# Kernel tuning notes

Hardware: AMD Instinct MI355X
Metric: run time of the kernel (lower is better)

Reference implementation:

```python
import jax, jax.numpy as jnp
import numpy as np

H = 8          # num heads
DK = 64        # d_model // H
D_MODEL = 512
WIN = 256


def setup_inputs() -> dict:
    key = jax.random.key(0)
    ks = jax.random.split(key, 12)
    B, S = 2, 2048
    mk = lambda k, shape, s=1.0: jax.random.normal(k, shape, dtype=jnp.float32) * s
    inp = {
        "query": mk(ks[0], (B, S, D_MODEL)),
        "key_in": mk(ks[1], (B, S, D_MODEL)),
        "value": mk(ks[2], (B, S, D_MODEL)),
        # nn.Linear(d_model, d_model) weights (out,in) and biases, x4
        "Wq": mk(ks[3], (D_MODEL, D_MODEL), 0.02), "bq": jnp.zeros((D_MODEL,), jnp.float32),
        "Wk": mk(ks[4], (D_MODEL, D_MODEL), 0.02), "bk": jnp.zeros((D_MODEL,), jnp.float32),
        "Wv": mk(ks[5], (D_MODEL, D_MODEL), 0.02), "bv": jnp.zeros((D_MODEL,), jnp.float32),
        "Wo": mk(ks[6], (D_MODEL, D_MODEL), 0.02), "bo": jnp.zeros((D_MODEL,), jnp.float32),
    }
    return inp


def reference(query, key_in, value, Wq, bq, Wk, bk, Wv, bv, Wo, bo):
    B, S, D = query.shape
    scale = np.float32(1.0 / np.sqrt(DK))

    def proj(x, W, b):
        # (B,S,D) -> (B,H,S,DK)
        return (x @ W.T + b).reshape(B, S, H, DK).transpose(0, 2, 1, 3)

    q = proj(query, Wq, bq)
    k = proj(key_in, Wk, bk)
    v = proj(value, Wv, bv)

    # Faithful to naive_masked_matmul: full (B,H,S,S) scores, with entries
    # OUTSIDE the sliding window left at exactly 0.0 (NOT -inf) before softmax.
    scores = jnp.einsum('bhid,bhjd->bhij', q, k) * scale
    idx = jnp.arange(S)
    band = jnp.abs(idx[:, None] - idx[None, :]) <= (WIN // 2)  # (S,S) bool
    scores = jnp.where(band, scores, jnp.float32(0.0))

    p_attn = jax.nn.softmax(scores, axis=-1)
    x = jnp.einsum('bhij,bhjd->bhid', p_attn, v)          # (B,H,S,DK)
    x = x.transpose(0, 2, 1, 3).reshape(B, S, D)          # (B,S,D)
    return x @ Wo.T + bo
```

## Files before the change

### kernel.cpp

```cpp
#include <hip/hip_runtime.h>
#include <hip/hip_bf16.h>

#define SS 2048
#define DD 512
#define HWIN 128

typedef __bf16 bf16x8 __attribute__((ext_vector_type(8)));
typedef unsigned short u16x8 __attribute__((ext_vector_type(8)));
typedef float f32x4 __attribute__((ext_vector_type(4)));

__device__ __forceinline__ unsigned short f2bf(float x) {
    unsigned u = __builtin_bit_cast(unsigned, x);
    return (unsigned short)((u + 0x7fffu + ((u >> 16) & 1u)) >> 16);
}
__device__ __forceinline__ float bf2f(unsigned short s) {
    unsigned u = ((unsigned)s) << 16;
    return __builtin_bit_cast(float, u);
}
__device__ __forceinline__ void split_bf(float x, unsigned short& h, unsigned short& l) {
    h = f2bf(x);
    l = f2bf(x - bf2f(h));
}
__device__ __forceinline__ void split8(float4 f0, float4 f1, u16x8& h, u16x8& l) {
    const float vals[8] = {f0.x, f0.y, f0.z, f0.w, f1.x, f1.y, f1.z, f1.w};
    #pragma unroll
    for (int i = 0; i < 8; ++i) {
        unsigned short hh, ll;
        split_bf(vals[i], hh, ll);
        h[i] = hh;
        l[i] = ll;
    }
}
__device__ __forceinline__ f32x4 mfma16(u16x8 a, u16x8 b, f32x4 c) {
    return __builtin_amdgcn_mfma_f32_16x16x32_bf16(
        __builtin_bit_cast(bf16x8, a), __builtin_bit_cast(bf16x8, b), c, 0, 0, 0);
}
__device__ __forceinline__ void gload16(const unsigned short* g, unsigned short* l) {
    __builtin_amdgcn_global_load_lds(
        (const __attribute__((address_space(1))) unsigned int*)g,
        (__attribute__((address_space(3))) unsigned int*)l, 16, 0, 0);
}

__global__ __launch_bounds__(256) void castW(
    const float* __restrict__ wq, const float* __restrict__ wk,
    const float* __restrict__ wv, const float* __restrict__ wo,
    unsigned short* __restrict__ WP, unsigned short* __restrict__ WoP)
{
    const size_t e0 = ((size_t)blockIdx.x * 256 + threadIdx.x) * 8;
    const float* src; size_t off; unsigned short* dst;
    if      (e0 < 262144) { src = wq; off = e0;          dst = WP + 2 * e0; }
    else if (e0 < 524288) { src = wk; off = e0 - 262144; dst = WP + 2 * e0; }
    else if (e0 < 786432) { src = wv; off = e0 - 524288; dst = WP + 2 * e0; }
    else                  { src = wo; off = e0 - 786432; dst = WoP + 2 * (e0 - 786432); }
    u16x8 h, l;
    split8(*(const float4*)(src + off), *(const float4*)(src + off + 4), h, l);
    *(u16x8*)(dst)     = h;
    *(u16x8*)(dst + 8) = l;
}

__global__ __launch_bounds__(256) void proj_gemm(
    const float* __restrict__ q, const float* __restrict__ k, const float* __restrict__ v,
    const unsigned short* __restrict__ WP,
    const float* __restrict__ bq, const float* __restrict__ bk, const float* __restrict__ bv,
    unsigned short* __restrict__ base,
    unsigned short* __restrict__ VTH, unsigned short* __restrict__ VTL)
{
    const int d = blockIdx.x;
    const int hi = d >> 6, low = d & 63;
    const int x = low >> 3, rsw = low & 7;
    const int g = hi * 8 + rsw;
    const int y = g / 3, z = g - y * 3;

    const float* A = (z == 0) ? q : ((z == 1) ? k : v);
    const unsigned short* Wp = WP + (size_t)z * 524288;
    const float* bias = (z == 0) ? bq : ((z == 1) ? bk : bv);
    unsigned short* OH = base + (size_t)z * 4194304;

    const int m0 = y * 128, n0 = x * 64;

    __shared__ unsigned short Ah[8 * 64 * 8], Al[8 * 64 * 8];
    __shared__ unsigned short Bh[4 * 64 * 8], Bl[4 * 64 * 8];

    const int tid = threadIdx.x, wave = tid >> 6, lane = tid & 63;
    const int lm = lane & 15, lq = lane >> 4;
    const int wm = wave >> 1, wn = wave & 1;
    const int kb = lq * 8;

    f32x4 acc[4][2] = {};

    const int ar0 = m0 + (wave * 2 + 0) * 16 + lm;
    const int ar1 = m0 + (wave * 2 + 1) * 16 + lm;
    const int br  = n0 + wave * 16 + lm;

    unsigned short* aD0h = &Ah[((wave * 2 + 0) * 64 + lane) * 8];
    unsigned short* aD1h = &Ah[((wave * 2 + 1) * 64 + lane) * 8];
    unsigned short* aD0l = &Al[((wave * 2 + 0) * 64 + lane) * 8];
    unsigned short* aD1l = &Al[((wave * 2 + 1) * 64 + lane) * 8];
    unsigned short* bDh  = &Bh[(wave * 64 + lane) * 8];
    unsigned short* bDl  = &Bl[(wave * 64 + lane) * 8];

    for (int k0 = 0; k0 < 512; k0 += 32) {
        const float* p0 = A + (size_t)ar0 * 512 + k0 + kb;
        const float4 f00 = *(const float4*)p0, f01 = *(const float4*)(p0 + 4);
        const float* p1 = A + (size_t)ar1 * 512 + k0 + kb;
        const float4 f10 = *(const float4*)p1, f11 = *(const float4*)(p1 + 4);

        __syncthreads();
        u16x8 a0h, a0l, a1h, a1l;
        split8(f00, f01, a0h, a0l);
        split8(f10, f11, a1h, a1l);
        *(u16x8*)aD0h = a0h; *(u16x8*)aD0l = a0l;
        *(u16x8*)aD1h = a1h; *(u16x8*)aD1l = a1l;
        {
            const unsigned short* pw = Wp + 2 * ((size_t)br * 512 + k0 + kb);
            gload16(pw,     bDh);
            gload16(pw + 8, bDl);
        }
        __syncthreads();

        u16x8 afh[4], afl[4], bfh[2], bfl[2];
        #pragma unroll
        for (int i = 0; i < 4; ++i) {
            afh[i] = *(const u16x8*)&Ah[((wm * 4 + i) * 64 + lane) * 8];
            afl[i] = *(const u16x8*)&Al[((wm * 4 + i) * 64 + lane) * 8];
        }
        #pragma unroll
        for (int j = 0; j < 2; ++j) {
            bfh[j] = *(const u16x8*)&Bh[((wn * 2 + j) * 64 + lane) * 8];
            bfl[j] = *(const u16x8*)&Bl[((wn * 2 + j) * 64 + lane) * 8];
        }
        #pragma unroll
        for (int i = 0; i < 4; ++i)
            #pragma unroll
            for (int j = 0; j < 2; ++j) {
                acc[i][j] = mfma16(afh[i], bfh[j], acc[i][j]);
                acc[i][j] = mfma16(afh[i], bfl[j], acc[i][j]);
                acc[i][j] = mfma16(afl[i], bfh[j], acc[i][j]);
            }
    }

    #pragma unroll
    for (int i = 0; i < 4; ++i)
        #pragma unroll
        for (int j = 0; j < 2; ++j) {
            const int col = n0 + (wn * 2 + j) * 16 + lm;
            const float bv_ = bias[col];
            #pragma unroll
            for (int r = 0; r < 4; ++r) {
                const int row = m0 + (wm * 4 + i) * 16 + lq * 4 + r;
                const float vv = acc[i][j][r] + bv_;
                unsigned short hh, ll;
                split_bf(vv, hh, ll);
                if (z == 2) {
                    const size_t vix =
                        (((size_t)(row >> 11) * 8 + (col >> 6)) * 64 + (col & 63)) * 2048
                        + (row & 2047);
                    VTH[vix] = hh;
                    VTL[vix] = ll;
                } else {
                    OH[(size_t)row * 512 + col] = hh;
                }
            }
        }
}

__global__ __launch_bounds__(256) void out_gemm(
    const unsigned short* __restrict__ XHg, const unsigned short* __restrict__ XLg,
    const unsigned short* __restrict__ WoP, const float* __restrict__ bo,
    float* __restrict__ O)
{
    const int gid = blockIdx.x;
    const int rr = gid & 7, hi = gid >> 3;
    const int nblk = hi & 7, mhi = hi >> 3;
    const int mblk = mhi * 8 + rr;
    const int m0 = mblk * 64, n0 = nblk * 64;

    __shared__ unsigned short Ah[8 * 64 * 8], Al[8 * 64 * 8];
    __shared__ unsigned short Bh[8 * 64 * 8], Bl[8 * 64 * 8];

    const int tid = threadIdx.x, wave = tid >> 6, lane = tid & 63;
    const int lm = lane & 15, lq = lane >> 4;
    const int kb = lq * 8;

    f32x4 acc[4] = {};

    const int arow = m0 + wave * 16 + lm;
    const int brow = n0 + wave * 16 + lm;

    for (int k0 = 0; k0 < 512; k0 += 64) {
        __syncthreads();
        #pragma unroll
        for (int s = 0; s < 2; ++s) {
            gload16(XHg + (size_t)arow * 512 + k0 + s * 32 + kb,
                    &Ah[((s * 4 + wave) * 64 + lane) * 8]);
            gload16(XLg + (size_t)arow * 512 + k0 + s * 32 + kb,
                    &Al[((s * 4 + wave) * 64 + lane) * 8]);
            const unsigned short* pw = WoP + 2 * ((size_t)brow * 512 + k0 + s * 32 + kb);
            gload16(pw,     &Bh[((s * 4 + wave) * 64 + lane) * 8]);
            gload16(pw + 8, &Bl[((s * 4 + wave) * 64 + lane) * 8]);
        }
        __syncthreads();

        #pragma unroll
        for (int s = 0; s < 2; ++s) {
            const u16x8 a_h = *(const u16x8*)&Ah[((s * 4 + wave) * 64 + lane) * 8];
            const u16x8 a_l = *(const u16x8*)&Al[((s * 4 + wave) * 64 + lane) * 8];
            #pragma unroll
            for (int j = 0; j < 4; ++j) {
                const u16x8 b_h = *(const u16x8*)&Bh[((s * 4 + j) * 64 + lane) * 8];
                const u16x8 b_l = *(const u16x8*)&Bl[((s * 4 + j) * 64 + lane) * 8];
                acc[j] = mfma16(a_h, b_h, acc[j]);
                acc[j] = mfma16(a_h, b_l, acc[j]);
                acc[j] = mfma16(a_l, b_h, acc[j]);
            }
        }
    }

    #pragma unroll
    for (int j = 0; j < 4; ++j) {
        const int col = n0 + j * 16 + lm;
        const float bv_ = bo[col];
        #pragma unroll
        for (int r = 0; r < 4; ++r) {
            const int row = m0 + wave * 16 + lq * 4 + r;
            O[(size_t)row * 512 + col] = acc[j][r] + bv_;
        }
    }
}

__global__ __launch_bounds__(256) void vsum_stage1(
    const unsigned short* __restrict__ VTH, const unsigned short* __restrict__ VTL,
    float* __restrict__ partial)
{
    const int bh = blockIdx.x, c = blockIdx.y;
    const int t = threadIdx.x, dd = t & 63, g = t >> 6;
    __shared__ float p[4][64];
    const size_t rb = ((size_t)bh * 64 + dd) * 2048 + c * 64 + g * 16;
    const u16x8 h0 = *(const u16x8*)(VTH + rb), h1 = *(const u16x8*)(VTH + rb + 8);
    const u16x8 l0 = *(const u16x8*)(VTL + rb), l1 = *(const u16x8*)(VTL + rb + 8);
    float acc = 0.f;
    #pragma unroll
    for (int i = 0; i < 8; ++i) acc += bf2f(h0[i]) + bf2f(l0[i]);
    #pragma unroll
    for (int i = 0; i < 8; ++i) acc += bf2f(h1[i]) + bf2f(l1[i]);
    p[g][dd] = acc;
    __syncthreads();
    if (t < 64)
        partial[((size_t)bh * 32 + c) * 64 + t] =
            p[0][t] + p[1][t] + p[2][t] + p[3][t];
}

__global__ __launch_bounds__(64) void vsum_stage2(
    const float* __restrict__ partial, float* __restrict__ VS)
{
    const int bh = blockIdx.x, dd = threadIdx.x;
    float acc = 0.f;
    #pragma unroll 8
    for (int c = 0; c < 32; ++c)
        acc += partial[((size_t)bh * 32 + c) * 64 + dd];
    VS[bh * 64 + dd] = acc;
}

__global__ __launch_bounds__(256) void attn_mfma(
    const unsigned short* __restrict__ QH, const unsigned short* __restrict__ KH,
    const unsigned short* __restrict__ VTH, const float* __restrict__ VS,
    unsigned short* __restrict__ XH, unsigned short* __restrict__ XL)
{
    const int dblk = blockIdx.x;
    const int bhi = dblk >> 8, blow = dblk & 255;
    const int xblk = blow >> 3, rrs = blow & 7;
    const int bh = bhi * 8 + rrs;
    const int h = bh & 7, b = bh >> 3;
    const int i0 = xblk * 64;
    const int tid = threadIdx.x, wave = tid >> 6, lane = tid & 63;
    const int lm = lane & 15, lq = lane >> 4;
    const int kb = lq * 8;

    __shared__ unsigned short KfH[8 * 64 * 8];
    __shared__ unsigned short VfH[8 * 64 * 8];
    __shared__ unsigned short Swh[64][72];

    const size_t qoff = ((size_t)(b * SS + i0 + wave * 16 + lm)) * DD + h * 64 + kb;
    const u16x8 aQ0h = *(const u16x8*)(QH + qoff);
    const u16x8 aQ1h = *(const u16x8*)(QH + qoff + 32);

    f32x4 oacc[4] = {};
    float dacc[4] = {0.f, 0.f, 0.f, 0.f};

    unsigned short* kDh0 = &KfH[((wave * 2 + 0) * 64 + lane) * 8];
    unsigned short* kDh1 = &KfH[((wave * 2 + 1) * 64 + lane) * 8];
    unsigned short* vDh0 = &VfH[((wave * 2 + 0) * 64 + lane) * 8];
    unsigned short* vDh1 = &VfH[((wave * 2 + 1) * 64 + lane) * 8];
    const size_t vrow = ((size_t)bh * 64 + wave * 16 + lm) * 2048;

    for (int jt = 0; jt < 5; ++jt) {
        const int jt0 = i0 - 128 + jt * 64;
        {
            const int jrow = jt0 + wave * 16 + lm;
            const int jrc = min(max(jrow, 0), SS - 1);
            const size_t kgb = ((size_t)(b * SS + jrc)) * DD + h * 64 + kb;
            gload16(KH + kgb,      kDh0);
            gload16(KH + kgb + 32, kDh1);
            const int j0c = min(max(jt0 + kb, 0), SS - 8);
            const int j1c = min(max(jt0 + 32 + kb, 0), SS - 8);
            gload16(VTH + vrow + j0c, vDh0);
            gload16(VTH + vrow + j1c, vDh1);
        }
        __syncthreads();

        #pragma unroll
        for (int js = 0; js < 4; ++js) {
            const int j0 = js * 16;
            const u16x8 bK0h = *(const u16x8*)&KfH[((js * 2 + 0) * 64 + lane) * 8];
            const u16x8 bK1h = *(const u16x8*)&KfH[((js * 2 + 1) * 64 + lane) * 8];
            f32x4 s = {0.f, 0.f, 0.f, 0.f};
            s = mfma16(aQ0h, bK0h, s);
            s = mfma16(aQ1h, bK1h, s);
            const int jg = jt0 + j0 + lm;
            const int iq = i0 + wave * 16 + lq * 4;
            #pragma unroll
            for (int r = 0; r < 4; ++r) {
                const int qi = iq + r;
                const bool in = (jg >= 0) && (jg < SS) &&
                                (jg >= qi - HWIN) && (jg <= qi + HWIN);
                const float w = in ? (__expf(s[r] * 0.125f) - 1.0f) : 0.0f;
                dacc[r] += w;
                Swh[wave * 16 + lq * 4 + r][j0 + lm] = f2bf(w);
            }
        }
        __syncthreads();

        const u16x8 aP0h = *(const u16x8*)&Swh[wave * 16 + lm][kb];
        const u16x8 aP1h = *(const u16x8*)&Swh[wave * 16 + lm][kb + 32];
        #pragma unroll
        for (int s4 = 0; s4 < 4; ++s4) {
            const u16x8 bV0h = *(const u16x8*)&VfH[((s4 * 2 + 0) * 64 + lane) * 8];
            const u16x8 bV1h = *(const u16x8*)&VfH[((s4 * 2 + 1) * 64 + lane) * 8];
            oacc[s4] = mfma16(aP0h, bV0h, oacc[s4]);
            oacc[s4] = mfma16(aP1h, bV1h, oacc[s4]);
        }
        __syncthreads();
    }

    #pragma unroll
    for (int r = 0; r < 4; ++r) {
        float v = dacc[r];
        v += __shfl_xor(v, 1);
        v += __shfl_xor(v, 2);
        v += __shfl_xor(v, 4);
        v += __shfl_xor(v, 8);
        dacc[r] = v + 2048.0f;
    }

    #pragma unroll
    for (int s4 = 0; s4 < 4; ++s4) {
        const float vsv = VS[bh * 64 + s4 * 16 + lm];
        #pragma unroll
        for (int r = 0; r < 4; ++r) {
            const int qrow = i0 + wave * 16 + lq * 4 + r;
            const float x = (oacc[s4][r] + vsv) / dacc[r];
            unsigned short xh, xl;
            split_bf(x, xh, xl);
            const size_t ix = ((size_t)(b * SS + qrow)) * DD + h * 64 + s4 * 16 + lm;
            XH[ix] = xh;
            XL[ix] = xl;
        }
    }
}

extern "C" void kernel_launch(void* const* d_in, const int* in_sizes, int n_in,
                              void* d_out, int out_size, void* d_ws, size_t ws_size,
                              hipStream_t stream)
{
    const float* query  = (const float*)d_in[0];
    const float* key_in = (const float*)d_in[1];
    const float* value  = (const float*)d_in[2];
    const float* Wq = (const float*)d_in[3]; const float* bq = (const float*)d_in[4];
    const float* Wk = (const float*)d_in[5]; const float* bk = (const float*)d_in[6];
    const float* Wv = (const float*)d_in[7]; const float* bv = (const float*)d_in[8];
    const float* Wo = (const float*)d_in[9]; const float* bo = (const float*)d_in[10];

    unsigned short* wsb = (unsigned short*)d_ws;
    unsigned short* QH  = wsb;
    unsigned short* KH  = wsb + 4194304;
    unsigned short* VTH = wsb + 8388608;
    unsigned short* VTL = wsb + 10485760;
    unsigned short* XH  = wsb + 12582912;
    unsigned short* XL  = wsb + 14680064;
    unsigned short* WP  = wsb + 16777216;
    unsigned short* WoP = wsb + 18350080;
    float* part = (float*)((char*)d_ws + 62914560);
    float* VSp  = (float*)((char*)d_ws + 63045632);

    castW<<<512, 256, 0, stream>>>(Wq, Wk, Wv, Wo, WP, WoP);

    proj_gemm<<<768, 256, 0, stream>>>(
        query, key_in, value, WP, bq, bk, bv, QH, VTH, VTL);

    vsum_stage1<<<dim3(16, 32), 256, 0, stream>>>(VTH, VTL, part);
    vsum_stage2<<<16, 64, 0, stream>>>(part, VSp);

    attn_mfma<<<512, 256, 0, stream>>>(QH, KH, VTH, VSp, XH, XL);

    out_gemm<<<512, 256, 0, stream>>>(XH, XL, WoP, bo, (float*)d_out);
}
```

Before: 167.7 us.

## Double-buffer LDS tiles in QKV projection and output GEMMs

```diff
diff --git a/kernel.cpp b/kernel.cpp
--- a/kernel.cpp
+++ b/kernel.cpp
@@ -78,8 +78,8 @@
 
     const int m0 = y * 128, n0 = x * 64;
 
-    __shared__ unsigned short Ah[8 * 64 * 8], Al[8 * 64 * 8];
-    __shared__ unsigned short Bh[4 * 64 * 8], Bl[4 * 64 * 8];
+    __shared__ unsigned short Ah[2 * 4096], Al[2 * 4096];
+    __shared__ unsigned short Bh[2 * 2048], Bl[2 * 2048];
 
     const int tid = threadIdx.x, wave = tid >> 6, lane = tid & 63;
     const int lm = lane & 15, lq = lane >> 4;
@@ -92,42 +92,52 @@
     const int ar1 = m0 + (wave * 2 + 1) * 16 + lm;
     const int br  = n0 + wave * 16 + lm;
 
-    unsigned short* aD0h = &Ah[((wave * 2 + 0) * 64 + lane) * 8];
-    unsigned short* aD1h = &Ah[((wave * 2 + 1) * 64 + lane) * 8];
-    unsigned short* aD0l = &Al[((wave * 2 + 0) * 64 + lane) * 8];
-    unsigned short* aD1l = &Al[((wave * 2 + 1) * 64 + lane) * 8];
-    unsigned short* bDh  = &Bh[(wave * 64 + lane) * 8];
-    unsigned short* bDl  = &Bl[(wave * 64 + lane) * 8];
-
-    for (int k0 = 0; k0 < 512; k0 += 32) {
-        const float* p0 = A + (size_t)ar0 * 512 + k0 + kb;
+    const int aoff0 = ((wave * 2 + 0) * 64 + lane) * 8;
+    const int aoff1 = ((wave * 2 + 1) * 64 + lane) * 8;
+    const int boff  = (wave * 64 + lane) * 8;
+
+    {
+        const float* p0 = A + (size_t)ar0 * 512 + kb;
         const float4 f00 = *(const float4*)p0, f01 = *(const float4*)(p0 + 4);
-        const float* p1 = A + (size_t)ar1 * 512 + k0 + kb;
+        const float* p1 = A + (size_t)ar1 * 512 + kb;
         const float4 f10 = *(const float4*)p1, f11 = *(const float4*)(p1 + 4);
-
-        __syncthreads();
-        u16x8 a0h, a0l, a1h, a1l;
-        split8(f00, f01, a0h, a0l);
-        split8(f10, f11, a1h, a1l);
-        *(u16x8*)aD0h = a0h; *(u16x8*)aD0l = a0l;
-        *(u16x8*)aD1h = a1h; *(u16x8*)aD1l = a1l;
-        {
-            const unsigned short* pw = Wp + 2 * ((size_t)br * 512 + k0 + kb);
-            gload16(pw,     bDh);
-            gload16(pw + 8, bDl);
-        }
-        __syncthreads();
+        const unsigned short* pw = Wp + 2 * ((size_t)br * 512 + kb);
+        gload16(pw,     &Bh[boff]);
+        gload16(pw + 8, &Bl[boff]);
+        u16x8 h0, l0, h1, l1;
+        split8(f00, f01, h0, l0);
+        split8(f10, f11, h1, l1);
+        *(u16x8*)&Ah[aoff0] = h0; *(u16x8*)&Al[aoff0] = l0;
+        *(u16x8*)&Ah[aoff1] = h1; *(u16x8*)&Al[aoff1] = l1;
+    }
+    __syncthreads();
+
+    int cur = 0;
+    for (int t = 0; t < 16; ++t) {
+        const int nxt = cur ^ 1;
+        const bool pf = (t < 15);
+        float4 f00, f01, f10, f11;
+        if (pf) {
+            const int k0n = (t + 1) * 32;
+            const float* p0 = A + (size_t)ar0 * 512 + k0n + kb;
+            f00 = *(const float4*)p0; f01 = *(const float4*)(p0 + 4);
+            const float* p1 = A + (size_t)ar1 * 512 + k0n + kb;
+            f10 = *(const float4*)p1; f11 = *(const float4*)(p1 + 4);
+            const unsigned short* pw = Wp + 2 * ((size_t)br * 512 + k0n + kb);
+            gload16(pw,     &Bh[nxt * 2048 + boff]);
+            gload16(pw + 8, &Bl[nxt * 2048 + boff]);
+        }
 
         u16x8 afh[4], afl[4], bfh[2], bfl[2];
         #pragma unroll
         for (int i = 0; i < 4; ++i) {
-            afh[i] = *(const u16x8*)&Ah[((wm * 4 + i) * 64 + lane) * 8];
-            afl[i] = *(const u16x8*)&Al[((wm * 4 + i) * 64 + lane) * 8];
+            afh[i] = *(const u16x8*)&Ah[cur * 4096 + ((wm * 4 + i) * 64 + lane) * 8];
+            afl[i] = *(const u16x8*)&Al[cur * 4096 + ((wm * 4 + i) * 64 + lane) * 8];
         }
         #pragma unroll
         for (int j = 0; j < 2; ++j) {
-            bfh[j] = *(const u16x8*)&Bh[((wn * 2 + j) * 64 + lane) * 8];
-            bfl[j] = *(const u16x8*)&Bl[((wn * 2 + j) * 64 + lane) * 8];
+            bfh[j] = *(const u16x8*)&Bh[cur * 2048 + ((wn * 2 + j) * 64 + lane) * 8];
+            bfl[j] = *(const u16x8*)&Bl[cur * 2048 + ((wn * 2 + j) * 64 + lane) * 8];
         }
         #pragma unroll
         for (int i = 0; i < 4; ++i)
@@ -137,6 +147,16 @@
                 acc[i][j] = mfma16(afh[i], bfl[j], acc[i][j]);
                 acc[i][j] = mfma16(afl[i], bfh[j], acc[i][j]);
             }
+
+        if (pf) {
+            u16x8 h0, l0, h1, l1;
+            split8(f00, f01, h0, l0);
+            split8(f10, f11, h1, l1);
+            *(u16x8*)&Ah[nxt * 4096 + aoff0] = h0; *(u16x8*)&Al[nxt * 4096 + aoff0] = l0;
+            *(u16x8*)&Ah[nxt * 4096 + aoff1] = h1; *(u16x8*)&Al[nxt * 4096 + aoff1] = l1;
+        }
+        __syncthreads();
+        cur = nxt;
     }
 
     #pragma unroll
@@ -175,8 +195,8 @@
     const int mblk = mhi * 8 + rr;
     const int m0 = mblk * 64, n0 = nblk * 64;
 
-    __shared__ unsigned short Ah[8 * 64 * 8], Al[8 * 64 * 8];
-    __shared__ unsigned short Bh[8 * 64 * 8], Bl[8 * 64 * 8];
+    __shared__ unsigned short Ah[2 * 4096], Al[2 * 4096];
+    __shared__ unsigned short Bh[2 * 4096], Bl[2 * 4096];
 
     const int tid = threadIdx.x, wave = tid >> 6, lane = tid & 63;
     const int lm = lane & 15, lq = lane >> 4;
@@ -187,33 +207,49 @@
     const int arow = m0 + wave * 16 + lm;
     const int brow = n0 + wave * 16 + lm;
 
-    for (int k0 = 0; k0 < 512; k0 += 64) {
-        __syncthreads();
+    #pragma unroll
+    for (int s = 0; s < 2; ++s) {
+        const int o = ((s * 4 + wave) * 64 + lane) * 8;
+        gload16(XHg + (size_t)arow * 512 + s * 32 + kb, &Ah[o]);
+        gload16(XLg + (size_t)arow * 512 + s * 32 + kb, &Al[o]);
+        const unsigned short* pw = WoP + 2 * ((size_t)brow * 512 + s * 32 + kb);
+        gload16(pw,     &Bh[o]);
+        gload16(pw + 8, &Bl[o]);
+    }
+    __syncthreads();
+
+    int cur = 0;
+    for (int t = 0; t < 8; ++t) {
+        const int nxt = cur ^ 1;
+        if (t < 7) {
+            const int k0n = (t + 1) * 64;
+            #pragma unroll
+            for (int s = 0; s < 2; ++s) {
+                const int o = nxt * 4096 + ((s * 4 + wave) * 64 + lane) * 8;
+                gload16(XHg + (size_t)arow * 512 + k0n + s * 32 + kb, &Ah[o]);
+                gload16(XLg + (size_t)arow * 512 + k0n + s * 32 + kb, &Al[o]);
+                const unsigned short* pw =
+                    WoP + 2 * ((size_t)brow * 512 + k0n + s * 32 + kb);
+                gload16(pw,     &Bh[o]);
+                gload16(pw + 8, &Bl[o]);
+            }
+        }
+
         #pragma unroll
         for (int s = 0; s < 2; ++s) {
-            gload16(XHg + (size_t)arow * 512 + k0 + s * 32 + kb,
-                    &Ah[((s * 4 + wave) * 64 + lane) * 8]);
-            gload16(XLg + (size_t)arow * 512 + k0 + s * 32 + kb,
-                    &Al[((s * 4 + wave) * 64 + lane) * 8]);
-            const unsigned short* pw = WoP + 2 * ((size_t)brow * 512 + k0 + s * 32 + kb);
-            gload16(pw,     &Bh[((s * 4 + wave) * 64 + lane) * 8]);
-            gload16(pw + 8, &Bl[((s * 4 + wave) * 64 + lane) * 8]);
-        }
-        __syncthreads();
-
-        #pragma unroll
-        for (int s = 0; s < 2; ++s) {
-            const u16x8 a_h = *(const u16x8*)&Ah[((s * 4 + wave) * 64 + lane) * 8];
-            const u16x8 a_l = *(const u16x8*)&Al[((s * 4 + wave) * 64 + lane) * 8];
+            const u16x8 a_h = *(const u16x8*)&Ah[cur * 4096 + ((s * 4 + wave) * 64 + lane) * 8];
+            const u16x8 a_l = *(const u16x8*)&Al[cur * 4096 + ((s * 4 + wave) * 64 + lane) * 8];
             #pragma unroll
             for (int j = 0; j < 4; ++j) {
-                const u16x8 b_h = *(const u16x8*)&Bh[((s * 4 + j) * 64 + lane) * 8];
-                const u16x8 b_l = *(const u16x8*)&Bl[((s * 4 + j) * 64 + lane) * 8];
+                const u16x8 b_h = *(const u16x8*)&Bh[cur * 4096 + ((s * 4 + j) * 64 + lane) * 8];
+                const u16x8 b_l = *(const u16x8*)&Bl[cur * 4096 + ((s * 4 + j) * 64 + lane) * 8];
                 acc[j] = mfma16(a_h, b_h, acc[j]);
                 acc[j] = mfma16(a_h, b_l, acc[j]);
                 acc[j] = mfma16(a_l, b_h, acc[j]);
             }
         }
+        __syncthreads();
+        cur = nxt;
     }
 
     #pragma unroll
```

Result: slower. 173.9 us (+3.7%).

## Replace LDS staging with direct global-to-register loads and register prefetch

Applied to the files above, without the earlier changes.

```diff
diff --git a/kernel.cpp b/kernel.cpp
--- a/kernel.cpp
+++ b/kernel.cpp
@@ -34,11 +34,6 @@
 __device__ __forceinline__ f32x4 mfma16(u16x8 a, u16x8 b, f32x4 c) {
     return __builtin_amdgcn_mfma_f32_16x16x32_bf16(
         __builtin_bit_cast(bf16x8, a), __builtin_bit_cast(bf16x8, b), c, 0, 0, 0);
-}
-__device__ __forceinline__ void gload16(const unsigned short* g, unsigned short* l) {
-    __builtin_amdgcn_global_load_lds(
-        (const __attribute__((address_space(1))) unsigned int*)g,
-        (__attribute__((address_space(3))) unsigned int*)l, 16, 0, 0);
 }
 
 __global__ __launch_bounds__(256) void castW(
@@ -78,9 +73,6 @@
 
     const int m0 = y * 128, n0 = x * 64;
 
-    __shared__ unsigned short Ah[8 * 64 * 8], Al[8 * 64 * 8];
-    __shared__ unsigned short Bh[4 * 64 * 8], Bl[4 * 64 * 8];
-
     const int tid = threadIdx.x, wave = tid >> 6, lane = tid & 63;
     const int lm = lane & 15, lq = lane >> 4;
     const int wm = wave >> 1, wn = wave & 1;
@@ -88,55 +80,61 @@
 
     f32x4 acc[4][2] = {};
 
-    const int ar0 = m0 + (wave * 2 + 0) * 16 + lm;
-    const int ar1 = m0 + (wave * 2 + 1) * 16 + lm;
-    const int br  = n0 + wave * 16 + lm;
-
-    unsigned short* aD0h = &Ah[((wave * 2 + 0) * 64 + lane) * 8];
-    unsigned short* aD1h = &Ah[((wave * 2 + 1) * 64 + lane) * 8];
-    unsigned short* aD0l = &Al[((wave * 2 + 0) * 64 + lane) * 8];
-    unsigned short* aD1l = &Al[((wave * 2 + 1) * 64 + lane) * 8];
-    unsigned short* bDh  = &Bh[(wave * 64 + lane) * 8];
-    unsigned short* bDl  = &Bl[(wave * 64 + lane) * 8];
-
-    for (int k0 = 0; k0 < 512; k0 += 32) {
-        const float* p0 = A + (size_t)ar0 * 512 + k0 + kb;
-        const float4 f00 = *(const float4*)p0, f01 = *(const float4*)(p0 + 4);
-        const float* p1 = A + (size_t)ar1 * 512 + k0 + kb;
-        const float4 f10 = *(const float4*)p1, f11 = *(const float4*)(p1 + 4);
-
-        __syncthreads();
-        u16x8 a0h, a0l, a1h, a1l;
-        split8(f00, f01, a0h, a0l);
-        split8(f10, f11, a1h, a1l);
-        *(u16x8*)aD0h = a0h; *(u16x8*)aD0l = a0l;
-        *(u16x8*)aD1h = a1h; *(u16x8*)aD1l = a1l;
-        {
-            const unsigned short* pw = Wp + 2 * ((size_t)br * 512 + k0 + kb);
-            gload16(pw,     bDh);
-            gload16(pw + 8, bDl);
-        }
-        __syncthreads();
-
-        u16x8 afh[4], afl[4], bfh[2], bfl[2];
+    const float* aRow[4];
+    const unsigned short* bRow[2];
+    #pragma unroll
+    for (int i = 0; i < 4; ++i)
+        aRow[i] = A + (size_t)(m0 + (wm * 4 + i) * 16 + lm) * 512 + kb;
+    #pragma unroll
+    for (int j = 0; j < 2; ++j)
+        bRow[j] = Wp + 2 * ((size_t)(n0 + (wn * 2 + j) * 16 + lm) * 512 + kb);
+
+    float4 cA[4][2];
+    u16x8 cBh[2], cBl[2];
+    #pragma unroll
+    for (int i = 0; i < 4; ++i) {
+        cA[i][0] = *(const float4*)(aRow[i]);
+        cA[i][1] = *(const float4*)(aRow[i] + 4);
+    }
+    #pragma unroll
+    for (int j = 0; j < 2; ++j) {
+        cBh[j] = *(const u16x8*)(bRow[j]);
+        cBl[j] = *(const u16x8*)(bRow[j] + 8);
+    }
+
+    for (int t = 0; t < 16; ++t) {
+        const int kn = (t == 15) ? 0 : (t + 1) * 32;
+
+        float4 nA[4][2];
+        u16x8 nBh[2], nBl[2];
         #pragma unroll
         for (int i = 0; i < 4; ++i) {
-            afh[i] = *(const u16x8*)&Ah[((wm * 4 + i) * 64 + lane) * 8];
-            afl[i] = *(const u16x8*)&Al[((wm * 4 + i) * 64 + lane) * 8];
+            nA[i][0] = *(const float4*)(aRow[i] + kn);
+            nA[i][1] = *(const float4*)(aRow[i] + kn + 4);
         }
         #pragma unroll
         for (int j = 0; j < 2; ++j) {
-            bfh[j] = *(const u16x8*)&Bh[((wn * 2 + j) * 64 + lane) * 8];
-            bfl[j] = *(const u16x8*)&Bl[((wn * 2 + j) * 64 + lane) * 8];
-        }
+            nBh[j] = *(const u16x8*)(bRow[j] + 2 * kn);
+            nBl[j] = *(const u16x8*)(bRow[j] + 2 * kn + 8);
+        }
+
+        u16x8 afh[4], afl[4];
+        #pragma unroll
+        for (int i = 0; i < 4; ++i) split8(cA[i][0], cA[i][1], afh[i], afl[i]);
+
         #pragma unroll
         for (int i = 0; i < 4; ++i)
             #pragma unroll
             for (int j = 0; j < 2; ++j) {
-                acc[i][j] = mfma16(afh[i], bfh[j], acc[i][j]);
-                acc[i][j] = mfma16(afh[i], bfl[j], acc[i][j]);
-                acc[i][j] = mfma16(afl[i], bfh[j], acc[i][j]);
+                acc[i][j] = mfma16(afh[i], cBh[j], acc[i][j]);
+                acc[i][j] = mfma16(afh[i], cBl[j], acc[i][j]);
+                acc[i][j] = mfma16(afl[i], cBh[j], acc[i][j]);
             }
+
+        #pragma unroll
+        for (int i = 0; i < 4; ++i) { cA[i][0] = nA[i][0]; cA[i][1] = nA[i][1]; }
+        #pragma unroll
+        for (int j = 0; j < 2; ++j) { cBh[j] = nBh[j]; cBl[j] = nBl[j]; }
     }
 
     #pragma unroll
@@ -175,44 +173,60 @@
     const int mblk = mhi * 8 + rr;
     const int m0 = mblk * 64, n0 = nblk * 64;
 
-    __shared__ unsigned short Ah[8 * 64 * 8], Al[8 * 64 * 8];
-    __shared__ unsigned short Bh[8 * 64 * 8], Bl[8 * 64 * 8];
-
     const int tid = threadIdx.x, wave = tid >> 6, lane = tid & 63;
     const int lm = lane & 15, lq = lane >> 4;
     const int kb = lq * 8;
 
     f32x4 acc[4] = {};
 
-    const int arow = m0 + wave * 16 + lm;
-    const int brow = n0 + wave * 16 + lm;
-
-    for (int k0 = 0; k0 < 512; k0 += 64) {
-        __syncthreads();
+    const unsigned short* aHrow = XHg + (size_t)(m0 + wave * 16 + lm) * 512 + kb;
+    const unsigned short* aLrow = XLg + (size_t)(m0 + wave * 16 + lm) * 512 + kb;
+    const unsigned short* bRow[4];
+    #pragma unroll
+    for (int j = 0; j < 4; ++j)
+        bRow[j] = WoP + 2 * ((size_t)(n0 + j * 16 + lm) * 512 + kb);
+
+    u16x8 cAh[2], cAl[2], cBh[2][4], cBl[2][4];
+    #pragma unroll
+    for (int s = 0; s < 2; ++s) {
+        cAh[s] = *(const u16x8*)(aHrow + s * 32);
+        cAl[s] = *(const u16x8*)(aLrow + s * 32);
+        #pragma unroll
+        for (int j = 0; j < 4; ++j) {
+            cBh[s][j] = *(const u16x8*)(bRow[j] + 2 * (s * 32));
+            cBl[s][j] = *(const u16x8*)(bRow[j] + 2 * (s * 32) + 8);
+        }
+    }
+
+    for (int t = 0; t < 8; ++t) {
+        const int kn = (t == 7) ? 0 : (t + 1) * 64;
+
+        u16x8 nAh[2], nAl[2], nBh[2][4], nBl[2][4];
         #pragma unroll
         for (int s = 0; s < 2; ++s) {
-            gload16(XHg + (size_t)arow * 512 + k0 + s * 32 + kb,
-                    &Ah[((s * 4 + wave) * 64 + lane) * 8]);
-            gload16(XLg + (size_t)arow * 512 + k0 + s * 32 + kb,
-                    &Al[((s * 4 + wave) * 64 + lane) * 8]);
-            const unsigned short* pw = WoP + 2 * ((size_t)brow * 512 + k0 + s * 32 + kb);
-            gload16(pw,     &Bh[((s * 4 + wave) * 64 + lane) * 8]);
-            gload16(pw + 8, &Bl[((s * 4 + wave) * 64 + lane) * 8]);
-        }
-        __syncthreads();
+            nAh[s] = *(const u16x8*)(aHrow + kn + s * 32);
+            nAl[s] = *(const u16x8*)(aLrow + kn + s * 32);
+            #pragma unroll
+            for (int j = 0; j < 4; ++j) {
+                nBh[s][j] = *(const u16x8*)(bRow[j] + 2 * (kn + s * 32));
+                nBl[s][j] = *(const u16x8*)(bRow[j] + 2 * (kn + s * 32) + 8);
+            }
+        }
+
+        #pragma unroll
+        for (int s = 0; s < 2; ++s)
+            #pragma unroll
+            for (int j = 0; j < 4; ++j) {
+                acc[j] = mfma16(cAh[s], cBh[s][j], acc[j]);
+                acc[j] = mfma16(cAh[s], cBl[s][j], acc[j]);
+                acc[j] = mfma16(cAl[s], cBh[s][j], acc[j]);
+            }
 
         #pragma unroll
         for (int s = 0; s < 2; ++s) {
-            const u16x8 a_h = *(const u16x8*)&Ah[((s * 4 + wave) * 64 + lane) * 8];
-            const u16x8 a_l = *(const u16x8*)&Al[((s * 4 + wave) * 64 + lane) * 8];
-            #pragma unroll
-            for (int j = 0; j < 4; ++j) {
-                const u16x8 b_h = *(const u16x8*)&Bh[((s * 4 + j) * 64 + lane) * 8];
-                const u16x8 b_l = *(const u16x8*)&Bl[((s * 4 + j) * 64 + lane) * 8];
-                acc[j] = mfma16(a_h, b_h, acc[j]);
-                acc[j] = mfma16(a_h, b_l, acc[j]);
-                acc[j] = mfma16(a_l, b_h, acc[j]);
-            }
+            cAh[s] = nAh[s]; cAl[s] = nAl[s];
+            #pragma unroll
+            for (int j = 0; j < 4; ++j) { cBh[s][j] = nBh[s][j]; cBl[s][j] = nBl[s][j]; }
         }
     }
 
@@ -276,8 +290,6 @@
     const int lm = lane & 15, lq = lane >> 4;
     const int kb = lq * 8;
 
-    __shared__ unsigned short KfH[8 * 64 * 8];
-    __shared__ unsigned short VfH[8 * 64 * 8];
     __shared__ unsigned short Swh[64][72];
 
     const size_t qoff = ((size_t)(b * SS + i0 + wave * 16 + lm)) * DD + h * 64 + kb;
@@ -287,32 +299,18 @@
     f32x4 oacc[4] = {};
     float dacc[4] = {0.f, 0.f, 0.f, 0.f};
 
-    unsigned short* kDh0 = &KfH[((wave * 2 + 0) * 64 + lane) * 8];
-    unsigned short* kDh1 = &KfH[((wave * 2 + 1) * 64 + lane) * 8];
-    unsigned short* vDh0 = &VfH[((wave * 2 + 0) * 64 + lane) * 8];
-    unsigned short* vDh1 = &VfH[((wave * 2 + 1) * 64 + lane) * 8];
-    const size_t vrow = ((size_t)bh * 64 + wave * 16 + lm) * 2048;
-
     for (int jt = 0; jt < 5; ++jt) {
         const int jt0 = i0 - 128 + jt * 64;
-        {
-            const int jrow = jt0 + wave * 16 + lm;
-            const int jrc = min(max(jrow, 0), SS - 1);
-            const size_t kgb = ((size_t)(b * SS + jrc)) * DD + h * 64 + kb;
-            gload16(KH + kgb,      kDh0);
-            gload16(KH + kgb + 32, kDh1);
-            const int j0c = min(max(jt0 + kb, 0), SS - 8);
-            const int j1c = min(max(jt0 + 32 + kb, 0), SS - 8);
-            gload16(VTH + vrow + j0c, vDh0);
-            gload16(VTH + vrow + j1c, vDh1);
-        }
-        __syncthreads();
+        const int j0c = min(max(jt0 + kb, 0), SS - 8);
+        const int j1c = min(max(jt0 + 32 + kb, 0), SS - 8);
 
         #pragma unroll
         for (int js = 0; js < 4; ++js) {
             const int j0 = js * 16;
-            const u16x8 bK0h = *(const u16x8*)&KfH[((js * 2 + 0) * 64 + lane) * 8];
-            const u16x8 bK1h = *(const u16x8*)&KfH[((js * 2 + 1) * 64 + lane) * 8];
+            const int jrc = min(max(jt0 + j0 + lm, 0), SS - 1);
+            const size_t kgb = ((size_t)(b * SS + jrc)) * DD + h * 64 + kb;
+            const u16x8 bK0h = *(const u16x8*)(KH + kgb);
+            const u16x8 bK1h = *(const u16x8*)(KH + kgb + 32);
             f32x4 s = {0.f, 0.f, 0.f, 0.f};
             s = mfma16(aQ0h, bK0h, s);
             s = mfma16(aQ1h, bK1h, s);
@@ -328,18 +326,17 @@
                 Swh[wave * 16 + lq * 4 + r][j0 + lm] = f2bf(w);
             }
         }
-        __syncthreads();
 
         const u16x8 aP0h = *(const u16x8*)&Swh[wave * 16 + lm][kb];
         const u16x8 aP1h = *(const u16x8*)&Swh[wave * 16 + lm][kb + 32];
         #pragma unroll
         for (int s4 = 0; s4 < 4; ++s4) {
-            const u16x8 bV0h = *(const u16x8*)&VfH[((s4 * 2 + 0) * 64 + lane) * 8];
-            const u16x8 bV1h = *(const u16x8*)&VfH[((s4 * 2 + 1) * 64 + lane) * 8];
+            const size_t vb = ((size_t)(bh * 64 + s4 * 16 + lm)) * 2048;
+            const u16x8 bV0h = *(const u16x8*)(VTH + vb + j0c);
+            const u16x8 bV1h = *(const u16x8*)(VTH + vb + j1c);
             oacc[s4] = mfma16(aP0h, bV0h, oacc[s4]);
             oacc[s4] = mfma16(aP1h, bV1h, oacc[s4]);
         }
-        __syncthreads();
     }
 
     #pragma unroll
```

Result: slower. 235.9 us (+40.7%).

## Double-buffer K/V tiles in attention and widen projection GEMM K-step

Applied to the files above, without the earlier changes.

```diff
diff --git a/kernel.cpp b/kernel.cpp
--- a/kernel.cpp
+++ b/kernel.cpp
@@ -78,8 +78,8 @@
 
     const int m0 = y * 128, n0 = x * 64;
 
-    __shared__ unsigned short Ah[8 * 64 * 8], Al[8 * 64 * 8];
-    __shared__ unsigned short Bh[4 * 64 * 8], Bl[4 * 64 * 8];
+    __shared__ unsigned short Ah[16 * 64 * 8], Al[16 * 64 * 8];
+    __shared__ unsigned short Bh[8 * 64 * 8],  Bl[8 * 64 * 8];
 
     const int tid = threadIdx.x, wave = tid >> 6, lane = tid & 63;
     const int lm = lane & 15, lq = lane >> 4;
@@ -92,51 +92,62 @@
     const int ar1 = m0 + (wave * 2 + 1) * 16 + lm;
     const int br  = n0 + wave * 16 + lm;
 
-    unsigned short* aD0h = &Ah[((wave * 2 + 0) * 64 + lane) * 8];
-    unsigned short* aD1h = &Ah[((wave * 2 + 1) * 64 + lane) * 8];
-    unsigned short* aD0l = &Al[((wave * 2 + 0) * 64 + lane) * 8];
-    unsigned short* aD1l = &Al[((wave * 2 + 1) * 64 + lane) * 8];
-    unsigned short* bDh  = &Bh[(wave * 64 + lane) * 8];
-    unsigned short* bDl  = &Bl[(wave * 64 + lane) * 8];
-
-    for (int k0 = 0; k0 < 512; k0 += 32) {
+    for (int k0 = 0; k0 < 512; k0 += 64) {
         const float* p0 = A + (size_t)ar0 * 512 + k0 + kb;
-        const float4 f00 = *(const float4*)p0, f01 = *(const float4*)(p0 + 4);
         const float* p1 = A + (size_t)ar1 * 512 + k0 + kb;
-        const float4 f10 = *(const float4*)p1, f11 = *(const float4*)(p1 + 4);
+        const float4 a00 = *(const float4*)(p0),      a01 = *(const float4*)(p0 + 4);
+        const float4 a02 = *(const float4*)(p0 + 32), a03 = *(const float4*)(p0 + 36);
+        const float4 a10 = *(const float4*)(p1),      a11 = *(const float4*)(p1 + 4);
+        const float4 a12 = *(const float4*)(p1 + 32), a13 = *(const float4*)(p1 + 36);
 
         __syncthreads();
-        u16x8 a0h, a0l, a1h, a1l;
-        split8(f00, f01, a0h, a0l);
-        split8(f10, f11, a1h, a1l);
-        *(u16x8*)aD0h = a0h; *(u16x8*)aD0l = a0l;
-        *(u16x8*)aD1h = a1h; *(u16x8*)aD1l = a1l;
         {
-            const unsigned short* pw = Wp + 2 * ((size_t)br * 512 + k0 + kb);
-            gload16(pw,     bDh);
-            gload16(pw + 8, bDl);
+            u16x8 h, l;
+            split8(a00, a01, h, l);
+            *(u16x8*)&Ah[((0 * 8 + wave * 2 + 0) * 64 + lane) * 8] = h;
+            *(u16x8*)&Al[((0 * 8 + wave * 2 + 0) * 64 + lane) * 8] = l;
+            split8(a02, a03, h, l);
+            *(u16x8*)&Ah[((1 * 8 + wave * 2 + 0) * 64 + lane) * 8] = h;
+            *(u16x8*)&Al[((1 * 8 + wave * 2 + 0) * 64 + lane) * 8] = l;
+            split8(a10, a11, h, l);
+            *(u16x8*)&Ah[((0 * 8 + wave * 2 + 1) * 64 + lane) * 8] = h;
+            *(u16x8*)&Al[((0 * 8 + wave * 2 + 1) * 64 + lane) * 8] = l;
+            split8(a12, a13, h, l);
+            *(u16x8*)&Ah[((1 * 8 + wave * 2 + 1) * 64 + lane) * 8] = h;
+            *(u16x8*)&Al[((1 * 8 + wave * 2 + 1) * 64 + lane) * 8] = l;
+        }
+        {
+            const unsigned short* pw0 = Wp + 2 * ((size_t)br * 512 + k0 + kb);
+            gload16(pw0,     &Bh[((0 * 4 + wave) * 64 + lane) * 8]);
+            gload16(pw0 + 8, &Bl[((0 * 4 + wave) * 64 + lane) * 8]);
+            const unsigned short* pw1 = Wp + 2 * ((size_t)br * 512 + k0 + 32 + kb);
+            gload16(pw1,     &Bh[((1 * 4 + wave) * 64 + lane) * 8]);
+            gload16(pw1 + 8, &Bl[((1 * 4 + wave) * 64 + lane) * 8]);
         }
         __syncthreads();
 
-        u16x8 afh[4], afl[4], bfh[2], bfl[2];
-        #pragma unroll
-        for (int i = 0; i < 4; ++i) {
-            afh[i] = *(const u16x8*)&Ah[((wm * 4 + i) * 64 + lane) * 8];
-            afl[i] = *(const u16x8*)&Al[((wm * 4 + i) * 64 + lane) * 8];
-        }
-        #pragma unroll
-        for (int j = 0; j < 2; ++j) {
-            bfh[j] = *(const u16x8*)&Bh[((wn * 2 + j) * 64 + lane) * 8];
-            bfl[j] = *(const u16x8*)&Bl[((wn * 2 + j) * 64 + lane) * 8];
-        }
-        #pragma unroll
-        for (int i = 0; i < 4; ++i)
+        #pragma unroll
+        for (int s = 0; s < 2; ++s) {
+            u16x8 afh[4], afl[4], bfh[2], bfl[2];
+            #pragma unroll
+            for (int i = 0; i < 4; ++i) {
+                afh[i] = *(const u16x8*)&Ah[((s * 8 + wm * 4 + i) * 64 + lane) * 8];
+                afl[i] = *(const u16x8*)&Al[((s * 8 + wm * 4 + i) * 64 + lane) * 8];
+            }
             #pragma unroll
             for (int j = 0; j < 2; ++j) {
-                acc[i][j] = mfma16(afh[i], bfh[j], acc[i][j]);
-                acc[i][j] = mfma16(afh[i], bfl[j], acc[i][j]);
-                acc[i][j] = mfma16(afl[i], bfh[j], acc[i][j]);
+                bfh[j] = *(const u16x8*)&Bh[((s * 4 + wn * 2 + j) * 64 + lane) * 8];
+                bfl[j] = *(const u16x8*)&Bl[((s * 4 + wn * 2 + j) * 64 + lane) * 8];
             }
+            #pragma unroll
+            for (int i = 0; i < 4; ++i)
+                #pragma unroll
+                for (int j = 0; j < 2; ++j) {
+                    acc[i][j] = mfma16(afh[i], bfh[j], acc[i][j]);
+                    acc[i][j] = mfma16(afh[i], bfl[j], acc[i][j]);
+                    acc[i][j] = mfma16(afl[i], bfh[j], acc[i][j]);
+                }
+        }
     }
 
     #pragma unroll
@@ -276,8 +287,8 @@
     const int lm = lane & 15, lq = lane >> 4;
     const int kb = lq * 8;
 
-    __shared__ unsigned short KfH[8 * 64 * 8];
-    __shared__ unsigned short VfH[8 * 64 * 8];
+    __shared__ unsigned short KfH[2 * 8 * 64 * 8];
+    __shared__ unsigned short VfH[2 * 8 * 64 * 8];
     __shared__ unsigned short Swh[64][72];
 
     const size_t qoff = ((size_t)(b * SS + i0 + wave * 16 + lm)) * DD + h * 64 + kb;
@@ -287,32 +298,37 @@
     f32x4 oacc[4] = {};
     float dacc[4] = {0.f, 0.f, 0.f, 0.f};
 
-    unsigned short* kDh0 = &KfH[((wave * 2 + 0) * 64 + lane) * 8];
-    unsigned short* kDh1 = &KfH[((wave * 2 + 1) * 64 + lane) * 8];
-    unsigned short* vDh0 = &VfH[((wave * 2 + 0) * 64 + lane) * 8];
-    unsigned short* vDh1 = &VfH[((wave * 2 + 1) * 64 + lane) * 8];
     const size_t vrow = ((size_t)bh * 64 + wave * 16 + lm) * 2048;
+    const int s0 = (wave * 2 + 0) * 64 * 8 + lane * 8;
+    const int s1 = (wave * 2 + 1) * 64 * 8 + lane * 8;
+
+    #define STAGE(jt_, bufsel)                                                  \
+    {                                                                           \
+        const int jt0_ = i0 - 128 + (jt_) * 64;                                 \
+        const int jrow = jt0_ + wave * 16 + lm;                                 \
+        const int jrc = min(max(jrow, 0), SS - 1);                              \
+        const size_t kgb = ((size_t)(b * SS + jrc)) * DD + h * 64 + kb;         \
+        gload16(KH + kgb,      &KfH[(bufsel) * 4096 + s0]);                     \
+        gload16(KH + kgb + 32, &KfH[(bufsel) * 4096 + s1]);                     \
+        const int j0c = min(max(jt0_ + kb, 0), SS - 8);                         \
+        const int j1c = min(max(jt0_ + 32 + kb, 0), SS - 8);                    \
+        gload16(VTH + vrow + j0c, &VfH[(bufsel) * 4096 + s0]);                  \
+        gload16(VTH + vrow + j1c, &VfH[(bufsel) * 4096 + s1]);                  \
+    }
+
+    STAGE(0, 0);
+    __syncthreads();
 
     for (int jt = 0; jt < 5; ++jt) {
+        const int buf = jt & 1;
+        if (jt < 4) STAGE(jt + 1, buf ^ 1);
         const int jt0 = i0 - 128 + jt * 64;
-        {
-            const int jrow = jt0 + wave * 16 + lm;
-            const int jrc = min(max(jrow, 0), SS - 1);
-            const size_t kgb = ((size_t)(b * SS + jrc)) * DD + h * 64 + kb;
-            gload16(KH + kgb,      kDh0);
-            gload16(KH + kgb + 32, kDh1);
-            const int j0c = min(max(jt0 + kb, 0), SS - 8);
-            const int j1c = min(max(jt0 + 32 + kb, 0), SS - 8);
-            gload16(VTH + vrow + j0c, vDh0);
-            gload16(VTH + vrow + j1c, vDh1);
-        }
-        __syncthreads();
 
         #pragma unroll
         for (int js = 0; js < 4; ++js) {
             const int j0 = js * 16;
-            const u16x8 bK0h = *(const u16x8*)&KfH[((js * 2 + 0) * 64 + lane) * 8];
-            const u16x8 bK1h = *(const u16x8*)&KfH[((js * 2 + 1) * 64 + lane) * 8];
+            const u16x8 bK0h = *(const u16x8*)&KfH[buf * 4096 + ((js * 2 + 0) * 64 + lane) * 8];
+            const u16x8 bK1h = *(const u16x8*)&KfH[buf * 4096 + ((js * 2 + 1) * 64 + lane) * 8];
             f32x4 s = {0.f, 0.f, 0.f, 0.f};
             s = mfma16(aQ0h, bK0h, s);
             s = mfma16(aQ1h, bK1h, s);
@@ -328,19 +344,19 @@
                 Swh[wave * 16 + lq * 4 + r][j0 + lm] = f2bf(w);
             }
         }
-        __syncthreads();
 
         const u16x8 aP0h = *(const u16x8*)&Swh[wave * 16 + lm][kb];
         const u16x8 aP1h = *(const u16x8*)&Swh[wave * 16 + lm][kb + 32];
         #pragma unroll
         for (int s4 = 0; s4 < 4; ++s4) {
-            const u16x8 bV0h = *(const u16x8*)&VfH[((s4 * 2 + 0) * 64 + lane) * 8];
-            const u16x8 bV1h = *(const u16x8*)&VfH[((s4 * 2 + 1) * 64 + lane) * 8];
+            const u16x8 bV0h = *(const u16x8*)&VfH[buf * 4096 + ((s4 * 2 + 0) * 64 + lane) * 8];
+            const u16x8 bV1h = *(const u16x8*)&VfH[buf * 4096 + ((s4 * 2 + 1) * 64 + lane) * 8];
             oacc[s4] = mfma16(aP0h, bV0h, oacc[s4]);
             oacc[s4] = mfma16(aP1h, bV1h, oacc[s4]);
         }
         __syncthreads();
     }
+    #undef STAGE
 
     #pragma unroll
     for (int r = 0; r < 4; ++r) {
```

After: 170.8 us. About the same (+1.8%).
